# Performance work log

Hardware: AMD Instinct MI355X
Metric: run time of the kernel (lower is better)

## Reference

```python
import jax, jax.numpy as jnp
import numpy as np

B, S, HID = 1, 2048, 4096
NH, NKV, HD = 32, 8, 128
ROPE_THETA = 10000.0


def setup_inputs() -> dict:
    key = jax.random.key(0)
    ks = jax.random.split(key, 6)
    hidden_states = jax.random.normal(ks[0], (B, S, HID), dtype=jnp.float32)
    # RoPE tables: inv_freq over half dims, duplicated (HF convention)
    inv_freq = 1.0 / (ROPE_THETA ** (jnp.arange(0, HD, 2, dtype=jnp.float32) / HD))
    freqs = jnp.arange(S, dtype=jnp.float32)[:, None] * inv_freq[None, :]  # [S, HD/2]
    emb = jnp.concatenate([freqs, freqs], axis=-1)  # [S, HD]
    cos = jnp.cos(emb)[None]  # [1, S, HD]
    sin = jnp.sin(emb)[None]
    # Additive causal mask [1, 1, S, S]
    neg = jnp.float32(-1e9)
    causal = jnp.triu(jnp.full((S, S), neg, dtype=jnp.float32), k=1)
    attention_mask = causal[None, None]
    scale = 0.02
    Wq = jax.random.normal(ks[1], (NH * HD, HID), dtype=jnp.float32) * scale
    Wk = jax.random.normal(ks[2], (NKV * HD, HID), dtype=jnp.float32) * scale
    Wv = jax.random.normal(ks[3], (NKV * HD, HID), dtype=jnp.float32) * scale
    Wo = jax.random.normal(ks[4], (HID, NH * HD), dtype=jnp.float32) * scale
    return {"hidden_states": hidden_states, "cos": cos, "sin": sin,
            "attention_mask": attention_mask, "Wq": Wq, "Wk": Wk, "Wv": Wv, "Wo": Wo}


def _rotate_half(x):
    x1, x2 = jnp.split(x, 2, axis=-1)
    return jnp.concatenate([-x2, x1], axis=-1)


def reference(hidden_states, cos, sin, attention_mask, Wq, Wk, Wv, Wo):
    bsz, q_len, _ = hidden_states.shape
    # Projections (nn.Linear: x @ W^T)
    q = jnp.einsum('bsh,dh->bsd', hidden_states, Wq).reshape(bsz, q_len, NH, HD).transpose(0, 2, 1, 3)
    k = jnp.einsum('bsh,dh->bsd', hidden_states, Wk).reshape(bsz, q_len, NKV, HD).transpose(0, 2, 1, 3)
    v = jnp.einsum('bsh,dh->bsd', hidden_states, Wv).reshape(bsz, q_len, NKV, HD).transpose(0, 2, 1, 3)
    # RoPE (cos/sin unsqueezed at dim 1)
    c = cos[:, None, :, :]
    s = sin[:, None, :, :]
    q = q * c + _rotate_half(q) * s
    k = k * c + _rotate_half(k) * s
    # repeat_kv for GQA
    n_rep = NH // NKV
    k = jnp.repeat(k, n_rep, axis=1)  # [b, NH, S, HD]
    v = jnp.repeat(v, n_rep, axis=1)
    scores = jnp.einsum('bhqd,bhkd->bhqk', q, k) / jnp.sqrt(jnp.float32(HD))
    scores = scores + attention_mask
    attn = jax.nn.softmax(scores.astype(jnp.float32), axis=-1).astype(q.dtype)
    out = jnp.einsum('bhqk,bhkd->bhqd', attn, v)  # [b, NH, S, HD]
    out = out.transpose(0, 2, 1, 3).reshape(bsz, q_len, NH * HD)
    return jnp.einsum('bsd,hd->bsh', out, Wo)
```

## Files before the change

### kernel.cpp

```cpp
#include <hip/hip_runtime.h>
#include <cstdint>

typedef __attribute__((ext_vector_type(8))) short short8;
typedef __attribute__((ext_vector_type(4))) float float4v;

#define S_LEN 2048
#define HIDDIM 4096

static __device__ __forceinline__ unsigned short f2bf(float f) {
  unsigned int u = __float_as_uint(f);
  unsigned int r = (u + 0x7FFFu + ((u >> 16) & 1u)) >> 16;
  return (unsigned short)r;
}
static __device__ __forceinline__ float bf2f(unsigned short h) {
  return __uint_as_float(((unsigned int)h) << 16);
}

static __device__ __forceinline__ void gload16(const void* gp, void* lp) {
  __builtin_amdgcn_global_load_lds(
      (const __attribute__((address_space(1))) void*)gp,
      (__attribute__((address_space(3))) void*)lp, 16, 0, 0);
}

__global__ __launch_bounds__(256) void cast_all(
    const float* __restrict__ s0, const float* __restrict__ s1,
    const float* __restrict__ s2, const float* __restrict__ s3,
    const float* __restrict__ s4,
    unsigned short* __restrict__ d0, unsigned short* __restrict__ d1,
    unsigned short* __restrict__ d2, unsigned short* __restrict__ d3,
    unsigned short* __restrict__ d4) {
  const long n0 = 2097152, n1 = 4194304, n2 = 1048576, n3 = 1048576, n4 = 4194304;
  const long total = n0 + n1 + n2 + n3 + n4;
  for (long i = (long)blockIdx.x * 256 + threadIdx.x; i < total;
       i += (long)gridDim.x * 256) {
    const float* src; unsigned short* dst; long j = i;
    if (j < n0) { src = s0; dst = d0; }
    else if ((j -= n0) < n1) { src = s1; dst = d1; }
    else if ((j -= n1) < n2) { src = s2; dst = d2; }
    else if ((j -= n2) < n3) { src = s3; dst = d3; }
    else { j -= n3; src = s4; dst = d4; }
    float4 v = reinterpret_cast<const float4*>(src)[j];
    ushort4 o;
    o.x = f2bf(v.x); o.y = f2bf(v.y); o.z = f2bf(v.z); o.w = f2bf(v.w);
    reinterpret_cast<ushort4*>(dst)[j] = o;
  }
}

__device__ __forceinline__ void gemm128_core(
    const unsigned short* __restrict__ A, const unsigned short* __restrict__ B,
    int mr0, int nc0, unsigned short* As, unsigned short* Bs,
    float4v acc[4][4]) {
  const int t = threadIdx.x;
  const int lane = t & 63;
  const int wid = t >> 6;
  const int wm = wid >> 1, wn = wid & 1;
  const int row = t >> 2, kc = (t & 3) * 8;

#pragma unroll
  for (int i = 0; i < 4; i++)
#pragma unroll
    for (int j = 0; j < 4; j++) acc[i][j] = (float4v){0.f, 0.f, 0.f, 0.f};

  auto stage = [&](int buf, int k0) {
    const unsigned short* ga = A + (long)(mr0 + row) * 4096 + k0 + kc;
    unsigned short* as = As + buf * 4096;
    gload16(ga, as + t * 8);
    gload16(ga + (long)64 * 4096, as + 2048 + t * 8);
    const unsigned short* gb = B + (long)(nc0 + row) * 4096 + k0 + kc;
    unsigned short* bs = Bs + buf * 4096;
    gload16(gb, bs + t * 8);
    gload16(gb + (long)64 * 4096, bs + 2048 + t * 8);
  };

  stage(0, 0);
  __syncthreads();
  for (int kt = 0; kt < 128; ++kt) {
    const int cur = kt & 1;
    if (kt + 1 < 128) stage(cur ^ 1, (kt + 1) * 32);
    const unsigned short* ab =
        As + cur * 4096 + (wm * 64 + (lane & 15)) * 32 + (lane >> 4) * 8;
    const unsigned short* bb =
        Bs + cur * 4096 + (wn * 64 + (lane & 15)) * 32 + (lane >> 4) * 8;
    short8 af[4], bfr[4];
#pragma unroll
    for (int i = 0; i < 4; i++) af[i] = *(const short8*)(ab + i * 512);
#pragma unroll
    for (int i = 0; i < 4; i++) bfr[i] = *(const short8*)(bb + i * 512);
#pragma unroll
    for (int mi = 0; mi < 4; mi++)
#pragma unroll
      for (int ni = 0; ni < 4; ni++)
        acc[mi][ni] = __builtin_amdgcn_mfma_f32_16x16x32_bf16(
            af[mi], bfr[ni], acc[mi][ni], 0, 0, 0);
    __syncthreads();
  }
}

__global__ __launch_bounds__(256) void gemm_qkv(
    const unsigned short* __restrict__ A,
    const unsigned short* __restrict__ Wq,
    const unsigned short* __restrict__ Wk,
    const unsigned short* __restrict__ Wv,
    unsigned short* __restrict__ Qb,
    unsigned short* __restrict__ Kb,
    unsigned short* __restrict__ Vt) {
  __shared__ unsigned short As[2 * 4096];
  __shared__ unsigned short Bs[2 * 4096];
  const int nb = blockIdx.x, mb = blockIdx.y;
  const unsigned short* Bp;
  int col0, mode;
  if (nb < 32)      { Bp = Wq; col0 = nb * 128;        mode = 0; }
  else if (nb < 40) { Bp = Wk; col0 = (nb - 32) * 128; mode = 1; }
  else              { Bp = Wv; col0 = (nb - 40) * 128; mode = 2; }
  const int mr0 = mb * 128;

  float4v acc[4][4];
  gemm128_core(A, Bp, mr0, col0, As, Bs, acc);

  const int lane = threadIdx.x & 63;
  const int wid = threadIdx.x >> 6;
  const int wm = wid >> 1, wn = wid & 1;
  const int lr = (lane >> 4) * 4, lc = lane & 15;
#pragma unroll
  for (int mi = 0; mi < 4; mi++)
#pragma unroll
    for (int ni = 0; ni < 4; ni++)
#pragma unroll
      for (int r = 0; r < 4; r++) {
        const int grow = mr0 + wm * 64 + mi * 16 + lr + r;
        const int gcol = col0 + wn * 64 + ni * 16 + lc;
        const unsigned short hv = f2bf(acc[mi][ni][r]);
        if (mode == 0)      Qb[(long)grow * 4096 + gcol] = hv;
        else if (mode == 1) Kb[(long)grow * 1024 + gcol] = hv;
        else                Vt[(long)gcol * 2048 + grow] = hv;
      }
}

__global__ __launch_bounds__(256) void gemm_out(
    const unsigned short* __restrict__ A,
    const unsigned short* __restrict__ W,
    float* __restrict__ C) {
  __shared__ unsigned short As[2 * 4096];
  __shared__ unsigned short Bs[2 * 4096];
  const int nb = blockIdx.x, mb = blockIdx.y;
  const int col0 = nb * 128, mr0 = mb * 128;
  float4v acc[4][4];
  gemm128_core(A, W, mr0, col0, As, Bs, acc);
  const int lane = threadIdx.x & 63;
  const int wid = threadIdx.x >> 6;
  const int wm = wid >> 1, wn = wid & 1;
  const int lr = (lane >> 4) * 4, lc = lane & 15;
#pragma unroll
  for (int mi = 0; mi < 4; mi++)
#pragma unroll
    for (int ni = 0; ni < 4; ni++)
#pragma unroll
      for (int r = 0; r < 4; r++) {
        const int grow = mr0 + wm * 64 + mi * 16 + lr + r;
        const int gcol = col0 + wn * 64 + ni * 16 + lc;
        C[(long)grow * 4096 + gcol] = acc[mi][ni][r];
      }
}

__global__ __launch_bounds__(256) void rope_kernel(
    unsigned short* __restrict__ Qb, unsigned short* __restrict__ Kb,
    const float* __restrict__ cosp, const float* __restrict__ sinp) {
  const long i = (long)blockIdx.x * 256 + threadIdx.x;
  unsigned short* buf;
  int nh;
  long j = i;
  if (j < 4194304) { buf = Qb; nh = 32; }
  else { j -= 4194304; buf = Kb; nh = 8; }
  const int d = (int)(j & 63);
  const long tmp = j >> 6;
  const int h = (int)(tmp % nh);
  const int s = (int)(tmp / nh);
  const long base = (long)s * nh * 128 + h * 128 + d;
  const float c = cosp[s * 128 + d];
  const float sn = sinp[s * 128 + d];
  const float x1 = bf2f(buf[base]);
  const float x2 = bf2f(buf[base + 64]);
  buf[base] = f2bf(x1 * c - x2 * sn);
  buf[base + 64] = f2bf(x2 * c + x1 * sn);
}

__global__ __launch_bounds__(256) void attn_kernel(
    const unsigned short* __restrict__ Q,
    const unsigned short* __restrict__ K,
    const unsigned short* __restrict__ Vt,
    unsigned short* __restrict__ AO) {
  __shared__ unsigned short Ks[2][8192];
  __shared__ unsigned short Vs[2][8192];
  __shared__ unsigned short P_lds[4][16][72];
  const int t = threadIdx.x, lane = t & 63, w = t >> 6;
  const int hq = blockIdx.x >> 4;
  const int pair = blockIdx.x & 15;
  const int hkv = hq >> 2;
  const int lc = lane & 15, lg = lane >> 4;
  const float scale = 0.08838834764831845f;

  auto stageK = [&](unsigned short* ks, int c0) {
#pragma unroll
    for (int i = 0; i < 4; i++) {
      const int o = (t + i * 256) * 16;
      const int row = o >> 8;
      const int scb = (o & 255) ^ ((row & 7) << 4);
      gload16(K + (long)(c0 + row) * 1024 + hkv * 128 + (scb >> 1),
              (char*)ks + o);
    }
  };
  auto stageV = [&](unsigned short* vs, int c0) {
#pragma unroll
    for (int i = 0; i < 4; i++) {
      const int o = (t + i * 256) * 16;
      const int row = o >> 7;
      const int scb = (o & 127) ^ ((row & 7) << 4);
      gload16(Vt + (long)(hkv * 128 + row) * 2048 + c0 + (scb >> 1),
              (char*)vs + o);
    }
  };

  for (int half = 0; half < 2; ++half) {
    const int qt = half ? pair : (31 - pair);
    const int qr0 = qt * 64 + w * 16;
    const int ntiles = qt + 1;

    short8 aq[4];
    const unsigned short* qbase = Q + (long)(qr0 + lc) * 4096 + hq * 128 + lg * 8;
#pragma unroll
    for (int kk = 0; kk < 4; kk++) aq[kk] = *(const short8*)(qbase + kk * 32);

    float m_i[4], l_i[4];
    float4v acc_o[8];
#pragma unroll
    for (int r = 0; r < 4; r++) { m_i[r] = -1e30f; l_i[r] = 0.f; }
#pragma unroll
    for (int n = 0; n < 8; n++) acc_o[n] = (float4v){0.f, 0.f, 0.f, 0.f};

    stageK(Ks[0], 0);
    stageV(Vs[0], 0);
    __syncthreads();

    for (int it = 0; it < ntiles; ++it) {
      const int cur = it & 1;
      if (it + 1 < ntiles) {
        stageK(Ks[cur ^ 1], (it + 1) * 64);
        stageV(Vs[cur ^ 1], (it + 1) * 64);
      }
      const char* ks = (const char*)Ks[cur];
      const char* vs = (const char*)Vs[cur];

      float4v accs[4];
#pragma unroll
      for (int n = 0; n < 4; n++) accs[n] = (float4v){0.f, 0.f, 0.f, 0.f};
#pragma unroll
      for (int n = 0; n < 4; n++) {
        const int row = n * 16 + lc;
        const int sx = (row & 7) << 4;
#pragma unroll
        for (int kk = 0; kk < 4; kk++) {
          short8 bk = *(const short8*)(ks + row * 256 + ((kk * 64 + lg * 16) ^ sx));
          accs[n] = __builtin_amdgcn_mfma_f32_16x16x32_bf16(aq[kk], bk, accs[n], 0, 0, 0);
        }
      }
      if (it == qt) {
#pragma unroll
        for (int n = 0; n < 4; n++) {
          const int gcol = it * 64 + n * 16 + lc;
#pragma unroll
          for (int r = 0; r < 4; r++) {
            const int grow = qr0 + lg * 4 + r;
            const float sv = accs[n][r] * scale;
            accs[n][r] = (gcol > grow) ? -1e30f : sv;
          }
        }
      } else {
#pragma unroll
        for (int n = 0; n < 4; n++)
#pragma unroll
          for (int r = 0; r < 4; r++) accs[n][r] *= scale;
      }
      float sc[4];
#pragma unroll
      for (int r = 0; r < 4; r++) {
        float vm = fmaxf(fmaxf(accs[0][r], accs[1][r]), fmaxf(accs[2][r], accs[3][r]));
#pragma unroll
        for (int x = 1; x < 16; x <<= 1) vm = fmaxf(vm, __shfl_xor(vm, x, 64));
        const float mn = fmaxf(m_i[r], vm);
        sc[r] = __expf(m_i[r] - mn);
        m_i[r] = mn;
        float rs = 0.f;
#pragma unroll
        for (int n = 0; n < 4; n++) {
          const float pv = __expf(accs[n][r] - mn);
          accs[n][r] = pv;
          rs += pv;
        }
#pragma unroll
        for (int x = 1; x < 16; x <<= 1) rs += __shfl_xor(rs, x, 64);
        l_i[r] = l_i[r] * sc[r] + rs;
      }
#pragma unroll
      for (int n = 0; n < 8; n++)
#pragma unroll
        for (int r = 0; r < 4; r++) acc_o[n][r] *= sc[r];
#pragma unroll
      for (int n = 0; n < 4; n++)
#pragma unroll
        for (int r = 0; r < 4; r++)
          P_lds[w][lg * 4 + r][n * 16 + lc] = f2bf(accs[n][r]);
#pragma unroll
      for (int kk = 0; kk < 2; kk++) {
        short8 ap = *(const short8*)&P_lds[w][lc][kk * 32 + lg * 8];
#pragma unroll
        for (int nd = 0; nd < 8; nd++) {
          const int row = nd * 16 + lc;
          const int cb = (kk * 64 + lg * 16) ^ ((row & 7) << 4);
          short8 bv = *(const short8*)(vs + row * 128 + cb);
          acc_o[nd] = __builtin_amdgcn_mfma_f32_16x16x32_bf16(ap, bv, acc_o[nd], 0, 0, 0);
        }
      }
      __syncthreads();
    }
#pragma unroll
    for (int nd = 0; nd < 8; nd++)
#pragma unroll
      for (int r = 0; r < 4; r++) {
        const float o = acc_o[nd][r] / l_i[r];
        const int grow = qr0 + lg * 4 + r;
        AO[(long)grow * 4096 + hq * 128 + nd * 16 + lc] = f2bf(o);
      }
  }
}

extern "C" void kernel_launch(void* const* d_in, const int* in_sizes, int n_in,
                              void* d_out, int out_size, void* d_ws, size_t ws_size,
                              hipStream_t stream) {
  const float* hidden = (const float*)d_in[0];
  const float* cosp   = (const float*)d_in[1];
  const float* sinp   = (const float*)d_in[2];
  const float* Wq = (const float*)d_in[4];
  const float* Wk = (const float*)d_in[5];
  const float* Wv = (const float*)d_in[6];
  const float* Wo = (const float*)d_in[7];
  float* out = (float*)d_out;

  char* ws = (char*)d_ws;
  unsigned short* hidB = (unsigned short*)(ws + 0);
  unsigned short* WqB  = (unsigned short*)(ws + 16777216);
  unsigned short* WkB  = (unsigned short*)(ws + 50331648);
  unsigned short* WvB  = (unsigned short*)(ws + 58720256);
  unsigned short* WoB  = (unsigned short*)(ws + 67108864);
  unsigned short* Qb   = (unsigned short*)(ws + 100663296);
  unsigned short* Kb   = (unsigned short*)(ws + 117440512);
  unsigned short* VtB  = (unsigned short*)(ws + 121634816);
  unsigned short* AO   = (unsigned short*)(ws + 125829120);

  cast_all<<<2048, 256, 0, stream>>>(hidden, Wq, Wk, Wv, Wo,
                                     hidB, WqB, WkB, WvB, WoB);
  gemm_qkv<<<dim3(48, 16), 256, 0, stream>>>(hidB, WqB, WkB, WvB, Qb, Kb, VtB);
  rope_kernel<<<20480, 256, 0, stream>>>(Qb, Kb, cosp, sinp);
  attn_kernel<<<512, 256, 0, stream>>>(Qb, Kb, VtB, AO);
  gemm_out<<<dim3(32, 16), 256, 0, stream>>>(AO, WoB, out);
}
```

Measured before the change: 574.0 us.

## Triple-buffer GEMM core with swizzled LDS layout and explicit vmcnt waits

Rewrites the shared bf16 GEMM core used by the QKV and output projections. It moves from double to triple buffering, keeping two tiles in flight via explicit s_waitcnt vmcnt and one barrier per iteration. It also XOR-swizzles the 16-byte chunks of the LDS layout to avoid bank conflicts on fragment reads, and raises wave priority around the MFMA block. The cost is 50% more LDS per block, which may lower occupancy, and the hand-written waitcnt counts must match the issued loads exactly.

```diff
diff --git a/kernel.cpp b/kernel.cpp
--- a/kernel.cpp
+++ b/kernel.cpp
@@ -46,53 +46,63 @@
   }
 }
 
-__device__ __forceinline__ void gemm128_core(
+__device__ __forceinline__ void gemm_core128(
     const unsigned short* __restrict__ A, const unsigned short* __restrict__ B,
     int mr0, int nc0, unsigned short* As, unsigned short* Bs,
     float4v acc[4][4]) {
-  const int t = threadIdx.x;
-  const int lane = t & 63;
-  const int wid = t >> 6;
-  const int wm = wid >> 1, wn = wid & 1;
-  const int row = t >> 2, kc = (t & 3) * 8;
+  const int t0 = threadIdx.x;
+  const int lane = t0 & 63;
+  const int w = t0 >> 6;
+  const int wm = w >> 1, wn = w & 1;
+
+  const int rowA = t0 >> 2;
+  const int gsw = (((t0 & 3) ^ (rowA & 3))) * 8;
+  const unsigned short* aSrc = A + (long)(mr0 + rowA) * 4096 + gsw;
+  const unsigned short* bSrc = B + (long)(nc0 + rowA) * 4096 + gsw;
+  unsigned short* aDst = As + t0 * 8;
+  unsigned short* bDst = Bs + t0 * 8;
+
+  const int lsw = ((((lane >> 4) ^ (lane & 3)) << 4) | ((lane & 15) << 6));
+  const char* aRd = (const char*)As + lsw + (wm << 12);
+  const char* bRd = (const char*)Bs + lsw + (wn << 12);
 
 #pragma unroll
   for (int i = 0; i < 4; i++)
 #pragma unroll
     for (int j = 0; j < 4; j++) acc[i][j] = (float4v){0.f, 0.f, 0.f, 0.f};
 
-  auto stage = [&](int buf, int k0) {
-    const unsigned short* ga = A + (long)(mr0 + row) * 4096 + k0 + kc;
-    unsigned short* as = As + buf * 4096;
-    gload16(ga, as + t * 8);
-    gload16(ga + (long)64 * 4096, as + 2048 + t * 8);
-    const unsigned short* gb = B + (long)(nc0 + row) * 4096 + k0 + kc;
-    unsigned short* bs = Bs + buf * 4096;
-    gload16(gb, bs + t * 8);
-    gload16(gb + (long)64 * 4096, bs + 2048 + t * 8);
+  auto stage = [&](int b, int kt) {
+    const int ko = kt * 32;
+    gload16(aSrc + ko, aDst + b * 4096);
+    gload16(aSrc + ko + 64 * 4096, aDst + b * 4096 + 2048);
+    gload16(bSrc + ko, bDst + b * 4096);
+    gload16(bSrc + ko + 64 * 4096, bDst + b * 4096 + 2048);
   };
-
   stage(0, 0);
-  __syncthreads();
-  for (int kt = 0; kt < 128; ++kt) {
-    const int cur = kt & 1;
-    if (kt + 1 < 128) stage(cur ^ 1, (kt + 1) * 32);
-    const unsigned short* ab =
-        As + cur * 4096 + (wm * 64 + (lane & 15)) * 32 + (lane >> 4) * 8;
-    const unsigned short* bb =
-        Bs + cur * 4096 + (wn * 64 + (lane & 15)) * 32 + (lane >> 4) * 8;
-    short8 af[4], bfr[4];
-#pragma unroll
-    for (int i = 0; i < 4; i++) af[i] = *(const short8*)(ab + i * 512);
-#pragma unroll
-    for (int i = 0; i < 4; i++) bfr[i] = *(const short8*)(bb + i * 512);
+  stage(1, 1);
+
+  for (int t = 0; t < 128; ++t) {
+    if (t < 127) asm volatile("s_waitcnt vmcnt(4)" ::: "memory");
+    else         asm volatile("s_waitcnt vmcnt(0)" ::: "memory");
+    __builtin_amdgcn_s_barrier();
+    __builtin_amdgcn_sched_barrier(0);
+    const int b = t % 3;
+    short8 af[4], bfv[4];
+#pragma unroll
+    for (int mi = 0; mi < 4; mi++)
+      af[mi] = *(const short8*)(aRd + b * 8192 + mi * 1024);
+#pragma unroll
+    for (int ni = 0; ni < 4; ni++)
+      bfv[ni] = *(const short8*)(bRd + b * 8192 + ni * 1024);
+    if (t + 2 < 128) stage((t + 2) % 3, t + 2);
+    __builtin_amdgcn_s_setprio(1);
 #pragma unroll
     for (int mi = 0; mi < 4; mi++)
 #pragma unroll
       for (int ni = 0; ni < 4; ni++)
         acc[mi][ni] = __builtin_amdgcn_mfma_f32_16x16x32_bf16(
-            af[mi], bfr[ni], acc[mi][ni], 0, 0, 0);
-    __syncthreads();
+            af[mi], bfv[ni], acc[mi][ni], 0, 0, 0);
+    __builtin_amdgcn_s_setprio(0);
   }
 }
 
@@ -104,8 +114,8 @@
     unsigned short* __restrict__ Qb,
     unsigned short* __restrict__ Kb,
     unsigned short* __restrict__ Vt) {
-  __shared__ unsigned short As[2 * 4096];
-  __shared__ unsigned short Bs[2 * 4096];
+  __shared__ unsigned short As[3 * 4096];
+  __shared__ unsigned short Bs[3 * 4096];
   const int nb = blockIdx.x, mb = blockIdx.y;
   const unsigned short* Bp;
   int col0, mode;
@@ -115,7 +125,7 @@
   const int mr0 = mb * 128;
 
   float4v acc[4][4];
-  gemm128_core(A, Bp, mr0, col0, As, Bs, acc);
+  gemm_core128(A, Bp, mr0, col0, As, Bs, acc);
 
   const int lane = threadIdx.x & 63;
   const int wid = threadIdx.x >> 6;
@@ -140,12 +150,12 @@
     const unsigned short* __restrict__ A,
     const unsigned short* __restrict__ W,
     float* __restrict__ C) {
-  __shared__ unsigned short As[2 * 4096];
-  __shared__ unsigned short Bs[2 * 4096];
+  __shared__ unsigned short As[3 * 4096];
+  __shared__ unsigned short Bs[3 * 4096];
   const int nb = blockIdx.x, mb = blockIdx.y;
   const int col0 = nb * 128, mr0 = mb * 128;
   float4v acc[4][4];
-  gemm128_core(A, W, mr0, col0, As, Bs, acc);
+  gemm_core128(A, W, mr0, col0, As, Bs, acc);
   const int lane = threadIdx.x & 63;
   const int wid = threadIdx.x >> 6;
   const int wm = wid >> 1, wn = wid & 1;
```

Result: faster. 530.8 us (-7.5%).
